# Kernel tuning notes

Measured on AMD Instinct MI355X. Metric: run time of the kernel, lower is better.

Reference implementation:

```python
import jax, jax.numpy as jnp
import numpy as np

N_NODES = 100000
N_EDGES = 640000
D_IN = 128
D_H = 128


def setup_inputs() -> dict:
    key = jax.random.key(0)
    ks = jax.random.split(key, 24)
    def W(k, shp):
        return jax.random.normal(k, shp, dtype=jnp.float32) * 0.05
    inp = {
        "x": jax.random.normal(ks[0], (N_NODES, D_IN), dtype=jnp.float32),
        "src": jax.random.randint(ks[1], (N_EDGES,), 0, N_NODES, dtype=jnp.int32),
        "dst": jax.random.randint(ks[2], (N_EDGES,), 0, N_NODES, dtype=jnp.int32),
        "neg_src": jax.random.randint(ks[3], (N_EDGES,), 0, N_NODES, dtype=jnp.int32),
        "neg_dst": jax.random.randint(ks[4], (N_EDGES,), 0, N_NODES, dtype=jnp.int32),
        # SAGEConv layer 1/2/3: fc_self weight, fc_neigh weight (stored [in,out]), bias
        "Ws1": W(ks[5], (D_IN, D_H)), "Wn1": W(ks[6], (D_IN, D_H)), "b1": jnp.zeros((D_H,), jnp.float32),
        "Ws2": W(ks[7], (D_H, D_H)), "Wn2": W(ks[8], (D_H, D_H)), "b2": jnp.zeros((D_H,), jnp.float32),
        "Ws3": W(ks[9], (D_H, D_H)), "Wn3": W(ks[10], (D_H, D_H)), "b3": jnp.zeros((D_H,), jnp.float32),
        # MLPPredictor: W1 [2h,h], W2 [h,1]
        "Wp1": W(ks[11], (2 * D_H, D_H)), "bp1": jnp.zeros((D_H,), jnp.float32),
        "Wp2": W(ks[12], (D_H, 1)), "bp2": jnp.zeros((1,), jnp.float32),
    }
    return inp


def _sage_mean(x, src, dst, Ws, Wn, b):
    # DGL SAGEConv 'mean': rst = fc_self(h) + fc_neigh(mean_{in-neighbors}(h)) + bias
    n = x.shape[0]
    msum = jax.ops.segment_sum(x[src], dst, num_segments=n)        # [N, d]
    deg = jax.ops.segment_sum(jnp.ones_like(src, dtype=x.dtype), dst, num_segments=n)
    mean = msum / jnp.clip(deg, 1.0)[:, None]                      # zero for isolated nodes
    return x @ Ws + mean @ Wn + b


def _edge_score(h, s, d, Wp1, bp1, Wp2, bp2):
    z = jnp.concatenate([h[s], h[d]], axis=1)                      # [E, 2h]
    return (jax.nn.relu(z @ Wp1 + bp1) @ Wp2 + bp2)[:, 0]          # [E]


def reference(x, src, dst, neg_src, neg_dst,
              Ws1, Wn1, b1, Ws2, Wn2, b2, Ws3, Wn3, b3,
              Wp1, bp1, Wp2, bp2):
    h = _sage_mean(x, src, dst, Ws1, Wn1, b1)
    h = _sage_mean(h, src, dst, Ws2, Wn2, b2)
    h = _sage_mean(h, src, dst, Ws3, Wn3, b3)
    pos = _edge_score(h, src, dst, Wp1, bp1, Wp2, bp2)
    neg = _edge_score(h, neg_src, neg_dst, Wp1, bp1, Wp2, bp2)
    return (pos, neg)
```

## Files before the change

### kernel.cpp

```cpp
#include <hip/hip_runtime.h>

#define N_NODES 100000
#define N_EDGES 640000
#define D 128
#define SCAN_TILE 1024
#define SCAN_BLOCKS ((N_NODES + SCAN_TILE - 1) / SCAN_TILE)

typedef __attribute__((ext_vector_type(8))) short bf16x8;
typedef __attribute__((ext_vector_type(4))) float f32x4;

__device__ __forceinline__ unsigned short f32_to_bf16(float f) {
  union { float f; unsigned int u; } v; v.f = f;
  unsigned int u = v.u;
  unsigned int r = (u + 0x7fffu + ((u >> 16) & 1u)) >> 16;
  return (unsigned short)r;
}
__device__ __forceinline__ float bf16_lo(unsigned int u) { return __uint_as_float(u << 16); }
__device__ __forceinline__ float bf16_hi(unsigned int u) { return __uint_as_float(u & 0xffff0000u); }

__global__ void zero_i32(int* __restrict__ p, int n) {
  int i = blockIdx.x * blockDim.x + threadIdx.x;
  if (i < n) p[i] = 0;
}

__global__ void f32_to_bf16_vec(const float* __restrict__ in, unsigned short* __restrict__ out, int n4) {
  int i = blockIdx.x * blockDim.x + threadIdx.x;
  if (i < n4) {
    float4 v = ((const float4*)in)[i];
    ushort4 o;
    o.x = f32_to_bf16(v.x); o.y = f32_to_bf16(v.y);
    o.z = f32_to_bf16(v.z); o.w = f32_to_bf16(v.w);
    ((ushort4*)out)[i] = o;
  }
}

__global__ void transpose_w(const float* __restrict__ W0, const float* __restrict__ W1,
                            const float* __restrict__ W2, const float* __restrict__ W3,
                            const float* __restrict__ W4, const float* __restrict__ W5,
                            const float* __restrict__ W6, const float* __restrict__ W7,
                            unsigned short* __restrict__ wt) {
  int id = blockIdx.x * 256 + threadIdx.x;
  int mat = id >> 14;
  int rem = id & 16383;
  int n = rem >> 7, k = rem & 127;
  const float* Wm = mat < 4 ? (mat < 2 ? (mat == 0 ? W0 : W1) : (mat == 2 ? W2 : W3))
                            : (mat < 6 ? (mat == 4 ? W4 : W5) : (mat == 6 ? W6 : W7));
  wt[id] = f32_to_bf16(Wm[k * D + n]);
}

__global__ void hist_kernel(const int* __restrict__ dst, int* __restrict__ deg, int E) {
  int i = blockIdx.x * blockDim.x + threadIdx.x;
  if (i < E) atomicAdd(&deg[dst[i]], 1);
}

__global__ void scan_blocksum(const int* __restrict__ deg, int* __restrict__ partial, int n) {
  __shared__ int lds[256];
  const int tid = threadIdx.x;
  const int base = blockIdx.x * SCAN_TILE + tid * 4;
  int s = 0;
#pragma unroll
  for (int j = 0; j < 4; ++j) {
    int i = base + j;
    if (i < n) s += deg[i];
  }
  lds[tid] = s;
  __syncthreads();
  for (int off = 128; off > 0; off >>= 1) {
    if (tid < off) lds[tid] += lds[tid + off];
    __syncthreads();
  }
  if (tid == 0) partial[blockIdx.x] = lds[0];
}

__global__ void scan_offsets(int* __restrict__ partial, int* __restrict__ row_start, int nb, int n) {
  __shared__ int lds[128];
  const int tid = threadIdx.x;
  int v = (tid < nb) ? partial[tid] : 0;
  lds[tid] = v;
  __syncthreads();
  for (int off = 1; off < 128; off <<= 1) {
    int t = (tid >= off) ? lds[tid - off] : 0;
    __syncthreads();
    lds[tid] += t;
    __syncthreads();
  }
  if (tid < nb) partial[tid] = (tid == 0) ? 0 : lds[tid - 1];
  if (tid == 0) row_start[n] = lds[nb - 1];
}

__global__ void scan_final(const int* __restrict__ deg, const int* __restrict__ partial,
                           int* __restrict__ row_start, int n) {
  __shared__ int lds[256];
  const int tid = threadIdx.x;
  const int base = blockIdx.x * SCAN_TILE + tid * 4;
  int d[4];
  int s = 0;
#pragma unroll
  for (int j = 0; j < 4; ++j) {
    int i = base + j;
    d[j] = (i < n) ? deg[i] : 0;
    s += d[j];
  }
  lds[tid] = s;
  __syncthreads();
  for (int off = 1; off < 256; off <<= 1) {
    int t = (tid >= off) ? lds[tid - off] : 0;
    __syncthreads();
    lds[tid] += t;
    __syncthreads();
  }
  int pre = partial[blockIdx.x] + lds[tid] - s;
#pragma unroll
  for (int j = 0; j < 4; ++j) {
    int i = base + j;
    if (i < n) {
      row_start[i] = pre;
      pre += d[j];
    }
  }
}

__global__ void fill_kernel(const int* __restrict__ src, const int* __restrict__ dst,
                            const int* __restrict__ row_start, int* __restrict__ cursor,
                            int* __restrict__ esrc, int E) {
  int i = blockIdx.x * blockDim.x + threadIdx.x;
  if (i < E) {
    int d = dst[i];
    int pos = atomicAdd(&cursor[d], 1);
    esrc[row_start[d] + pos] = src[i];
  }
}

__global__ void aggregate_bf16(const unsigned short* __restrict__ h, const int* __restrict__ row_start,
                               const int* __restrict__ esrc, unsigned short* __restrict__ mean, int n) {
  const int t = blockIdx.x * blockDim.x + threadIdx.x;
  const int node = t >> 4;
  const int fl = threadIdx.x & 15;
  if (node >= n) return;
  const int s0 = row_start[node], s1 = row_start[node + 1];
  float acc[8] = {0.f, 0.f, 0.f, 0.f, 0.f, 0.f, 0.f, 0.f};
  int e = s0;
  for (; e + 4 <= s1; e += 4) {
    int i0 = esrc[e], i1 = esrc[e + 1], i2 = esrc[e + 2], i3 = esrc[e + 3];
    uint4 r0 = *(const uint4*)(h + (size_t)i0 * D + fl * 8);
    uint4 r1 = *(const uint4*)(h + (size_t)i1 * D + fl * 8);
    uint4 r2 = *(const uint4*)(h + (size_t)i2 * D + fl * 8);
    uint4 r3 = *(const uint4*)(h + (size_t)i3 * D + fl * 8);
    acc[0] += bf16_lo(r0.x); acc[1] += bf16_hi(r0.x);
    acc[2] += bf16_lo(r0.y); acc[3] += bf16_hi(r0.y);
    acc[4] += bf16_lo(r0.z); acc[5] += bf16_hi(r0.z);
    acc[6] += bf16_lo(r0.w); acc[7] += bf16_hi(r0.w);
    acc[0] += bf16_lo(r1.x); acc[1] += bf16_hi(r1.x);
    acc[2] += bf16_lo(r1.y); acc[3] += bf16_hi(r1.y);
    acc[4] += bf16_lo(r1.z); acc[5] += bf16_hi(r1.z);
    acc[6] += bf16_lo(r1.w); acc[7] += bf16_hi(r1.w);
    acc[0] += bf16_lo(r2.x); acc[1] += bf16_hi(r2.x);
    acc[2] += bf16_lo(r2.y); acc[3] += bf16_hi(r2.y);
    acc[4] += bf16_lo(r2.z); acc[5] += bf16_hi(r2.z);
    acc[6] += bf16_lo(r2.w); acc[7] += bf16_hi(r2.w);
    acc[0] += bf16_lo(r3.x); acc[1] += bf16_hi(r3.x);
    acc[2] += bf16_lo(r3.y); acc[3] += bf16_hi(r3.y);
    acc[4] += bf16_lo(r3.z); acc[5] += bf16_hi(r3.z);
    acc[6] += bf16_lo(r3.w); acc[7] += bf16_hi(r3.w);
  }
  for (; e < s1; ++e) {
    int s = esrc[e];
    uint4 raw = *(const uint4*)(h + (size_t)s * D + fl * 8);
    acc[0] += bf16_lo(raw.x); acc[1] += bf16_hi(raw.x);
    acc[2] += bf16_lo(raw.y); acc[3] += bf16_hi(raw.y);
    acc[4] += bf16_lo(raw.z); acc[5] += bf16_hi(raw.z);
    acc[6] += bf16_lo(raw.w); acc[7] += bf16_hi(raw.w);
  }
  const float inv = 1.0f / (float)max(s1 - s0, 1);
  uint4 o;
  o.x = (unsigned)f32_to_bf16(acc[0] * inv) | ((unsigned)f32_to_bf16(acc[1] * inv) << 16);
  o.y = (unsigned)f32_to_bf16(acc[2] * inv) | ((unsigned)f32_to_bf16(acc[3] * inv) << 16);
  o.z = (unsigned)f32_to_bf16(acc[4] * inv) | ((unsigned)f32_to_bf16(acc[5] * inv) << 16);
  o.w = (unsigned)f32_to_bf16(acc[6] * inv) | ((unsigned)f32_to_bf16(acc[7] * inv) << 16);
  *(uint4*)(mean + (size_t)node * D + fl * 8) = o;
}

template <int NCHUNK, bool FP32OUT>
__global__ __launch_bounds__(256) void gemm_mfma(
    const unsigned short* __restrict__ in0, const unsigned short* __restrict__ in1,
    const unsigned short* __restrict__ Wt0, const unsigned short* __restrict__ Wt1,
    const float* __restrict__ bias, void* __restrict__ out, int M) {
  __shared__ unsigned short wl[128][136];
  const int tid = threadIdx.x;
  const int lane = tid & 63;
  const int wave = tid >> 6;
  const int m0 = blockIdx.x * 64 + wave * 16;
  const int row = lane & 15;
  const int q = lane >> 4;
  const int mload = min(m0 + row, M - 1);

  bf16x8 afrag[NCHUNK * 4];
#pragma unroll
  for (int s = 0; s < NCHUNK * 4; ++s) {
    const unsigned short* srcp = (NCHUNK == 2 && s >= 4) ? in1 : in0;
    afrag[s] = *reinterpret_cast<const bf16x8*>(srcp + (size_t)mload * D + (s & 3) * 32 + q * 8);
  }
  f32x4 acc[8];
#pragma unroll
  for (int t = 0; t < 8; ++t) acc[t] = (f32x4){0.f, 0.f, 0.f, 0.f};

  for (int c = 0; c < NCHUNK; ++c) {
    const unsigned short* wsrc = (c == 0) ? Wt0 : Wt1;
    if (c) __syncthreads();
#pragma unroll
    for (int i = 0; i < 8; ++i) {
      int seg = i * 256 + tid;
      int r = seg >> 4;
      int o = (seg & 15) * 8;
      *reinterpret_cast<bf16x8*>(&wl[r][o]) =
          *reinterpret_cast<const bf16x8*>(wsrc + r * D + o);
    }
    __syncthreads();
#pragma unroll
    for (int s = 0; s < 4; ++s) {
#pragma unroll
      for (int t = 0; t < 8; ++t) {
        const int n = t * 16 + row;
        bf16x8 b = *reinterpret_cast<const bf16x8*>(&wl[n][s * 32 + q * 8]);
        acc[t] = __builtin_amdgcn_mfma_f32_16x16x32_bf16(afrag[c * 4 + s], b, acc[t], 0, 0, 0);
      }
    }
  }

#pragma unroll
  for (int t = 0; t < 8; ++t) {
    const int col = t * 16 + row;
    const float bv = bias ? bias[col] : 0.f;
#pragma unroll
    for (int r = 0; r < 4; ++r) {
      int m = m0 + q * 4 + r;
      if (m < M) {
        float v = acc[t][r] + bv;
        if (FP32OUT)
          ((float*)out)[(size_t)m * D + col] = v;
        else
          ((unsigned short*)out)[(size_t)m * D + col] = f32_to_bf16(v);
      }
    }
  }
}

__global__ void edge_score_fused(const unsigned short* __restrict__ A, const unsigned short* __restrict__ B,
                                 const int* __restrict__ ps, const int* __restrict__ pd,
                                 const int* __restrict__ ns, const int* __restrict__ nd,
                                 const float* __restrict__ Wp2, const float* __restrict__ bp2,
                                 float* __restrict__ out, int E) {
  const int t = blockIdx.x * blockDim.x + threadIdx.x;
  const int e = t >> 4;
  const int fl = threadIdx.x & 15;
  if (e >= E) return;
  const int si = ps[e], di = pd[e];
  const int nsi = ns[e], ndi = nd[e];
  uint4 ra = *(const uint4*)(A + (size_t)si * D + fl * 8);
  uint4 rb = *(const uint4*)(B + (size_t)di * D + fl * 8);
  uint4 rna = *(const uint4*)(A + (size_t)nsi * D + fl * 8);
  uint4 rnb = *(const uint4*)(B + (size_t)ndi * D + fl * 8);
  float4 w0 = *(const float4*)(Wp2 + fl * 8);
  float4 w1 = *(const float4*)(Wp2 + fl * 8 + 4);

  float pp =
      fmaxf(bf16_lo(ra.x) + bf16_lo(rb.x), 0.f) * w0.x +
      fmaxf(bf16_hi(ra.x) + bf16_hi(rb.x), 0.f) * w0.y +
      fmaxf(bf16_lo(ra.y) + bf16_lo(rb.y), 0.f) * w0.z +
      fmaxf(bf16_hi(ra.y) + bf16_hi(rb.y), 0.f) * w0.w +
      fmaxf(bf16_lo(ra.z) + bf16_lo(rb.z), 0.f) * w1.x +
      fmaxf(bf16_hi(ra.z) + bf16_hi(rb.z), 0.f) * w1.y +
      fmaxf(bf16_lo(ra.w) + bf16_lo(rb.w), 0.f) * w1.z +
      fmaxf(bf16_hi(ra.w) + bf16_hi(rb.w), 0.f) * w1.w;
  float pn =
      fmaxf(bf16_lo(rna.x) + bf16_lo(rnb.x), 0.f) * w0.x +
      fmaxf(bf16_hi(rna.x) + bf16_hi(rnb.x), 0.f) * w0.y +
      fmaxf(bf16_lo(rna.y) + bf16_lo(rnb.y), 0.f) * w0.z +
      fmaxf(bf16_hi(rna.y) + bf16_hi(rnb.y), 0.f) * w0.w +
      fmaxf(bf16_lo(rna.z) + bf16_lo(rnb.z), 0.f) * w1.x +
      fmaxf(bf16_hi(rna.z) + bf16_hi(rnb.z), 0.f) * w1.y +
      fmaxf(bf16_lo(rna.w) + bf16_lo(rnb.w), 0.f) * w1.z +
      fmaxf(bf16_hi(rna.w) + bf16_hi(rnb.w), 0.f) * w1.w;

  pp += __shfl_xor(pp, 1);  pn += __shfl_xor(pn, 1);
  pp += __shfl_xor(pp, 2);  pn += __shfl_xor(pn, 2);
  pp += __shfl_xor(pp, 4);  pn += __shfl_xor(pn, 4);
  pp += __shfl_xor(pp, 8);  pn += __shfl_xor(pn, 8);
  if (fl == 0) {
    float b = bp2[0];
    out[e] = pp + b;
    out[E + e] = pn + b;
  }
}

extern "C" void kernel_launch(void* const* d_in, const int* in_sizes, int n_in,
                              void* d_out, int out_size, void* d_ws, size_t ws_size,
                              hipStream_t stream) {
  const float* x = (const float*)d_in[0];
  const int* src = (const int*)d_in[1];
  const int* dst = (const int*)d_in[2];
  const int* nsrc = (const int*)d_in[3];
  const int* ndst = (const int*)d_in[4];
  const float* Ws1 = (const float*)d_in[5];
  const float* Wn1 = (const float*)d_in[6];
  const float* b1 = (const float*)d_in[7];
  const float* Ws2 = (const float*)d_in[8];
  const float* Wn2 = (const float*)d_in[9];
  const float* b2 = (const float*)d_in[10];
  const float* Ws3 = (const float*)d_in[11];
  const float* Wn3 = (const float*)d_in[12];
  const float* b3 = (const float*)d_in[13];
  const float* Wp1 = (const float*)d_in[14];
  const float* bp1 = (const float*)d_in[15];
  const float* Wp2 = (const float*)d_in[16];
  const float* bp2 = (const float*)d_in[17];
  float* out = (float*)d_out;

  char* ws = (char*)d_ws;
  size_t off = 0;
  auto alloc = [&](size_t bytes) -> void* {
    void* p = ws + off;
    off += (bytes + 255) & ~(size_t)255;
    return p;
  };
  const size_t NODE_F32 = sizeof(float) * (size_t)N_NODES * D;
  char* region0 = (char*)alloc(NODE_F32);
  char* region1 = (char*)alloc(NODE_F32);
  char* region2 = (char*)alloc(NODE_F32);
  int* row_start = (int*)alloc(sizeof(int) * (N_NODES + 1));
  int* deg = (int*)alloc(sizeof(int) * N_NODES * 2);
  int* cursor = deg + N_NODES;
  int* esrc = (int*)alloc(sizeof(int) * N_EDGES);
  int* partial = (int*)alloc(sizeof(int) * 128);
  unsigned short* wt = (unsigned short*)alloc(sizeof(unsigned short) * 8 * D * D);
  (void)ws_size;

  unsigned short* xb = (unsigned short*)region0;
  unsigned short* meanb = xb + (size_t)N_NODES * D;
  unsigned short* hA = (unsigned short*)region1;
  unsigned short* hB = hA + (size_t)N_NODES * D;
  unsigned short* Ab = (unsigned short*)region2;
  unsigned short* Bb = Ab + (size_t)N_NODES * D;

  f32_to_bf16_vec<<<(N_NODES * D / 4 + 255) / 256, 256, 0, stream>>>(x, xb, N_NODES * D / 4);
  transpose_w<<<512, 256, 0, stream>>>(Ws1, Wn1, Ws2, Wn2, Ws3, Wn3, Wp1, Wp1 + D * D, wt);

  zero_i32<<<(2 * N_NODES + 255) / 256, 256, 0, stream>>>(deg, 2 * N_NODES);
  hist_kernel<<<(N_EDGES + 255) / 256, 256, 0, stream>>>(dst, deg, N_EDGES);
  scan_blocksum<<<SCAN_BLOCKS, 256, 0, stream>>>(deg, partial, N_NODES);
  scan_offsets<<<1, 128, 0, stream>>>(partial, row_start, SCAN_BLOCKS, N_NODES);
  scan_final<<<SCAN_BLOCKS, 256, 0, stream>>>(deg, partial, row_start, N_NODES);
  fill_kernel<<<(N_EDGES + 255) / 256, 256, 0, stream>>>(src, dst, row_start, cursor, esrc, N_EDGES);

  const int aggBlocks = (N_NODES * 16 + 255) / 256;
  const int gemmBlocks = (N_NODES + 63) / 64;
  const int edgeBlocks = (N_EDGES * 16) / 256;

  aggregate_bf16<<<aggBlocks, 256, 0, stream>>>(xb, row_start, esrc, meanb, N_NODES);
  gemm_mfma<2, false><<<gemmBlocks, 256, 0, stream>>>(xb, meanb, wt, wt + 16384, b1, hA, N_NODES);
  aggregate_bf16<<<aggBlocks, 256, 0, stream>>>(hA, row_start, esrc, meanb, N_NODES);
  gemm_mfma<2, false><<<gemmBlocks, 256, 0, stream>>>(hA, meanb, wt + 2 * 16384, wt + 3 * 16384, b2, hB, N_NODES);
  aggregate_bf16<<<aggBlocks, 256, 0, stream>>>(hB, row_start, esrc, meanb, N_NODES);
  gemm_mfma<2, false><<<gemmBlocks, 256, 0, stream>>>(hB, meanb, wt + 4 * 16384, wt + 5 * 16384, b3, hA, N_NODES);
  gemm_mfma<1, false><<<gemmBlocks, 256, 0, stream>>>(hA, nullptr, wt + 6 * 16384, nullptr, bp1, Ab, N_NODES);
  gemm_mfma<1, false><<<gemmBlocks, 256, 0, stream>>>(hA, nullptr, wt + 7 * 16384, nullptr, nullptr, Bb, N_NODES);
  edge_score_fused<<<edgeBlocks, 256, 0, stream>>>(Ab, Bb, src, dst, nsrc, ndst, Wp2, bp2, out, N_EDGES);
}
```

Before: 507.5 us.

## Sort edge scoring by destination via dual CSR and fuse predictor GEMMs

The CSR build now covers both positive and negative edges, bucketing negative edges by destination in a second node range and recording an inverse permutation. Edge scoring walks edges in destination-sorted order, so the B-row gathers hit the same or nearby rows, which should improve cache locality. Scores go to a temporary buffer and a permute kernel scatters them back to original order and adds the bias. The two predictor GEMMs are merged into one kernel that loads the A fragments once. In exchange the sort pass does more atomics and writes more memory, and the permute kernel is an extra launch.

```diff
diff --git a/kernel.cpp b/kernel.cpp
--- a/kernel.cpp
+++ b/kernel.cpp
@@ -3,8 +3,10 @@
 #define N_NODES 100000
 #define N_EDGES 640000
 #define D 128
-#define SCAN_TILE 1024
-#define SCAN_BLOCKS ((N_NODES + SCAN_TILE - 1) / SCAN_TILE)
+#define N2 (2 * N_NODES)
+#define E2 (2 * N_EDGES)
+#define SCAN_TILE 2048
+#define SCAN_BLOCKS ((N2 + SCAN_TILE - 1) / SCAN_TILE)
 
 typedef __attribute__((ext_vector_type(8))) short bf16x8;
 typedef __attribute__((ext_vector_type(4))) float f32x4;
@@ -48,18 +50,22 @@
   wt[id] = f32_to_bf16(Wm[k * D + n]);
 }
 
-__global__ void hist_kernel(const int* __restrict__ dst, int* __restrict__ deg, int E) {
+__global__ void hist_dual(const int* __restrict__ dst, const int* __restrict__ ndst,
+                          int* __restrict__ deg, int E) {
   int i = blockIdx.x * blockDim.x + threadIdx.x;
-  if (i < E) atomicAdd(&deg[dst[i]], 1);
+  if (i < E) {
+    atomicAdd(&deg[dst[i]], 1);
+    atomicAdd(&deg[N_NODES + ndst[i]], 1);
+  }
 }
 
 __global__ void scan_blocksum(const int* __restrict__ deg, int* __restrict__ partial, int n) {
   __shared__ int lds[256];
   const int tid = threadIdx.x;
-  const int base = blockIdx.x * SCAN_TILE + tid * 4;
+  const int base = blockIdx.x * SCAN_TILE + tid * 8;
   int s = 0;
 #pragma unroll
-  for (int j = 0; j < 4; ++j) {
+  for (int j = 0; j < 8; ++j) {
     int i = base + j;
     if (i < n) s += deg[i];
   }
@@ -92,11 +98,11 @@
                            int* __restrict__ row_start, int n) {
   __shared__ int lds[256];
   const int tid = threadIdx.x;
-  const int base = blockIdx.x * SCAN_TILE + tid * 4;
-  int d[4];
+  const int base = blockIdx.x * SCAN_TILE + tid * 8;
+  int d[8];
   int s = 0;
 #pragma unroll
-  for (int j = 0; j < 4; ++j) {
+  for (int j = 0; j < 8; ++j) {
     int i = base + j;
     d[j] = (i < n) ? deg[i] : 0;
     s += d[j];
@@ -111,7 +117,7 @@
   }
   int pre = partial[blockIdx.x] + lds[tid] - s;
 #pragma unroll
-  for (int j = 0; j < 4; ++j) {
+  for (int j = 0; j < 8; ++j) {
     int i = base + j;
     if (i < n) {
       row_start[i] = pre;
@@ -120,14 +126,25 @@
   }
 }
 
-__global__ void fill_kernel(const int* __restrict__ src, const int* __restrict__ dst,
-                            const int* __restrict__ row_start, int* __restrict__ cursor,
-                            int* __restrict__ esrc, int E) {
+__global__ void fill_dual(const int* __restrict__ src, const int* __restrict__ dst,
+                          const int* __restrict__ nsrc, const int* __restrict__ ndst,
+                          const int* __restrict__ row_start, int* __restrict__ cursor,
+                          int* __restrict__ esrc, int* __restrict__ edst,
+                          int* __restrict__ inv, int E) {
   int i = blockIdx.x * blockDim.x + threadIdx.x;
   if (i < E) {
     int d = dst[i];
-    int pos = atomicAdd(&cursor[d], 1);
-    esrc[row_start[d] + pos] = src[i];
+    int p = atomicAdd(&cursor[d], 1);
+    int slot = row_start[d] + p;
+    esrc[slot] = src[i];
+    edst[slot] = d;
+    inv[i] = slot;
+    int dn = N_NODES + ndst[i];
+    int p2 = atomicAdd(&cursor[dn], 1);
+    int slot2 = row_start[dn] + p2;
+    esrc[slot2] = nsrc[i];
+    edst[slot2] = ndst[i];
+    inv[E + i] = slot2;
   }
 }
 
@@ -245,52 +262,114 @@
   }
 }
 
-__global__ void edge_score_fused(const unsigned short* __restrict__ A, const unsigned short* __restrict__ B,
-                                 const int* __restrict__ ps, const int* __restrict__ pd,
-                                 const int* __restrict__ ns, const int* __restrict__ nd,
-                                 const float* __restrict__ Wp2, const float* __restrict__ bp2,
-                                 float* __restrict__ out, int E) {
+__global__ __launch_bounds__(256) void gemm_pred(
+    const unsigned short* __restrict__ in,
+    const unsigned short* __restrict__ WtA, const unsigned short* __restrict__ WtB,
+    const float* __restrict__ biasA,
+    unsigned short* __restrict__ outA, unsigned short* __restrict__ outB, int M) {
+  __shared__ unsigned short wl[128][136];
+  const int tid = threadIdx.x;
+  const int lane = tid & 63;
+  const int wave = tid >> 6;
+  const int m0 = blockIdx.x * 64 + wave * 16;
+  const int row = lane & 15;
+  const int q = lane >> 4;
+  const int mload = min(m0 + row, M - 1);
+
+  bf16x8 afrag[4];
+#pragma unroll
+  for (int s = 0; s < 4; ++s)
+    afrag[s] = *reinterpret_cast<const bf16x8*>(in + (size_t)mload * D + s * 32 + q * 8);
+
+  f32x4 acc[8];
+  for (int pass = 0; pass < 2; ++pass) {
+    const unsigned short* wsrc = pass ? WtB : WtA;
+    if (pass) __syncthreads();
+#pragma unroll
+    for (int i = 0; i < 8; ++i) {
+      int seg = i * 256 + tid;
+      int r = seg >> 4;
+      int o = (seg & 15) * 8;
+      *reinterpret_cast<bf16x8*>(&wl[r][o]) =
+          *reinterpret_cast<const bf16x8*>(wsrc + r * D + o);
+    }
+    __syncthreads();
+#pragma unroll
+    for (int t = 0; t < 8; ++t) acc[t] = (f32x4){0.f, 0.f, 0.f, 0.f};
+#pragma unroll
+    for (int s = 0; s < 4; ++s) {
+#pragma unroll
+      for (int t = 0; t < 8; ++t) {
+        const int n = t * 16 + row;
+        bf16x8 b = *reinterpret_cast<const bf16x8*>(&wl[n][s * 32 + q * 8]);
+        acc[t] = __builtin_amdgcn_mfma_f32_16x16x32_bf16(afrag[s], b, acc[t], 0, 0, 0);
+      }
+    }
+    unsigned short* outp = pass ? outB : outA;
+#pragma unroll
+    for (int t = 0; t < 8; ++t) {
+      const int col = t * 16 + row;
+      const float bv = pass ? 0.f : biasA[col];
+#pragma unroll
+      for (int r = 0; r < 4; ++r) {
+        int m = m0 + q * 4 + r;
+        if (m < M) outp[(size_t)m * D + col] = f32_to_bf16(acc[t][r] + bv);
+      }
+    }
+    if (pass == 0) __syncthreads();
+  }
+}
+
+__global__ void edge_score_csr(const unsigned short* __restrict__ A, const unsigned short* __restrict__ B,
+                               const int* __restrict__ esrc, const int* __restrict__ edst,
+                               const float* __restrict__ Wp2, float* __restrict__ tmp, int npairs) {
   const int t = blockIdx.x * blockDim.x + threadIdx.x;
-  const int e = t >> 4;
+  const int g = t >> 4;
   const int fl = threadIdx.x & 15;
-  if (e >= E) return;
-  const int si = ps[e], di = pd[e];
-  const int nsi = ns[e], ndi = nd[e];
-  uint4 ra = *(const uint4*)(A + (size_t)si * D + fl * 8);
-  uint4 rb = *(const uint4*)(B + (size_t)di * D + fl * 8);
-  uint4 rna = *(const uint4*)(A + (size_t)nsi * D + fl * 8);
-  uint4 rnb = *(const uint4*)(B + (size_t)ndi * D + fl * 8);
+  if (g >= npairs) return;
+  const int sl = 2 * g;
+  const int s0 = esrc[sl], d0 = edst[sl];
+  const int s1 = esrc[sl + 1], d1 = edst[sl + 1];
+  uint4 ra0 = *(const uint4*)(A + (size_t)s0 * D + fl * 8);
+  uint4 rb0 = *(const uint4*)(B + (size_t)d0 * D + fl * 8);
+  uint4 ra1 = *(const uint4*)(A + (size_t)s1 * D + fl * 8);
+  uint4 rb1 = *(const uint4*)(B + (size_t)d1 * D + fl * 8);
   float4 w0 = *(const float4*)(Wp2 + fl * 8);
   float4 w1 = *(const float4*)(Wp2 + fl * 8 + 4);
 
-  float pp =
-      fmaxf(bf16_lo(ra.x) + bf16_lo(rb.x), 0.f) * w0.x +
-      fmaxf(bf16_hi(ra.x) + bf16_hi(rb.x), 0.f) * w0.y +
-      fmaxf(bf16_lo(ra.y) + bf16_lo(rb.y), 0.f) * w0.z +
-      fmaxf(bf16_hi(ra.y) + bf16_hi(rb.y), 0.f) * w0.w +
-      fmaxf(bf16_lo(ra.z) + bf16_lo(rb.z), 0.f) * w1.x +
-      fmaxf(bf16_hi(ra.z) + bf16_hi(rb.z), 0.f) * w1.y +
-      fmaxf(bf16_lo(ra.w) + bf16_lo(rb.w), 0.f) * w1.z +
-      fmaxf(bf16_hi(ra.w) + bf16_hi(rb.w), 0.f) * w1.w;
-  float pn =
-      fmaxf(bf16_lo(rna.x) + bf16_lo(rnb.x), 0.f) * w0.x +
-      fmaxf(bf16_hi(rna.x) + bf16_hi(rnb.x), 0.f) * w0.y +
-      fmaxf(bf16_lo(rna.y) + bf16_lo(rnb.y), 0.f) * w0.z +
-      fmaxf(bf16_hi(rna.y) + bf16_hi(rnb.y), 0.f) * w0.w +
-      fmaxf(bf16_lo(rna.z) + bf16_lo(rnb.z), 0.f) * w1.x +
-      fmaxf(bf16_hi(rna.z) + bf16_hi(rnb.z), 0.f) * w1.y +
-      fmaxf(bf16_lo(rna.w) + bf16_lo(rnb.w), 0.f) * w1.z +
-      fmaxf(bf16_hi(rna.w) + bf16_hi(rnb.w), 0.f) * w1.w;
-
-  pp += __shfl_xor(pp, 1);  pn += __shfl_xor(pn, 1);
-  pp += __shfl_xor(pp, 2);  pn += __shfl_xor(pn, 2);
-  pp += __shfl_xor(pp, 4);  pn += __shfl_xor(pn, 4);
-  pp += __shfl_xor(pp, 8);  pn += __shfl_xor(pn, 8);
+  float p0 =
+      fmaxf(bf16_lo(ra0.x) + bf16_lo(rb0.x), 0.f) * w0.x +
+      fmaxf(bf16_hi(ra0.x) + bf16_hi(rb0.x), 0.f) * w0.y +
+      fmaxf(bf16_lo(ra0.y) + bf16_lo(rb0.y), 0.f) * w0.z +
+      fmaxf(bf16_hi(ra0.y) + bf16_hi(rb0.y), 0.f) * w0.w +
+      fmaxf(bf16_lo(ra0.z) + bf16_lo(rb0.z), 0.f) * w1.x +
+      fmaxf(bf16_hi(ra0.z) + bf16_hi(rb0.z), 0.f) * w1.y +
+      fmaxf(bf16_lo(ra0.w) + bf16_lo(rb0.w), 0.f) * w1.z +
+      fmaxf(bf16_hi(ra0.w) + bf16_hi(rb0.w), 0.f) * w1.w;
+  float p1 =
+      fmaxf(bf16_lo(ra1.x) + bf16_lo(rb1.x), 0.f) * w0.x +
+      fmaxf(bf16_hi(ra1.x) + bf16_hi(rb1.x), 0.f) * w0.y +
+      fmaxf(bf16_lo(ra1.y) + bf16_lo(rb1.y), 0.f) * w0.z +
+      fmaxf(bf16_hi(ra1.y) + bf16_hi(rb1.y), 0.f) * w0.w +
+      fmaxf(bf16_lo(ra1.z) + bf16_lo(rb1.z), 0.f) * w1.x +
+      fmaxf(bf16_hi(ra1.z) + bf16_hi(rb1.z), 0.f) * w1.y +
+      fmaxf(bf16_lo(ra1.w) + bf16_lo(rb1.w), 0.f) * w1.z +
+      fmaxf(bf16_hi(ra1.w) + bf16_hi(rb1.w), 0.f) * w1.w;
+
+  p0 += __shfl_xor(p0, 1);  p1 += __shfl_xor(p1, 1);
+  p0 += __shfl_xor(p0, 2);  p1 += __shfl_xor(p1, 2);
+  p0 += __shfl_xor(p0, 4);  p1 += __shfl_xor(p1, 4);
+  p0 += __shfl_xor(p0, 8);  p1 += __shfl_xor(p1, 8);
   if (fl == 0) {
-    float b = bp2[0];
-    out[e] = pp + b;
-    out[E + e] = pn + b;
-  }
+    tmp[sl] = p0;
+    tmp[sl + 1] = p1;
+  }
+}
+
+__global__ void permute_out(const float* __restrict__ tmp, const int* __restrict__ inv,
+                            const float* __restrict__ bp2, float* __restrict__ out, int n) {
+  int i = blockIdx.x * blockDim.x + threadIdx.x;
+  if (i < n) out[i] = tmp[inv[i]] + bp2[0];
 }
 
 extern "C" void kernel_launch(void* const* d_in, const int* in_sizes, int n_in,
@@ -326,12 +405,13 @@
   const size_t NODE_F32 = sizeof(float) * (size_t)N_NODES * D;
   char* region0 = (char*)alloc(NODE_F32);
   char* region1 = (char*)alloc(NODE_F32);
-  char* region2 = (char*)alloc(NODE_F32);
-  int* row_start = (int*)alloc(sizeof(int) * (N_NODES + 1));
-  int* deg = (int*)alloc(sizeof(int) * N_NODES * 2);
-  int* cursor = deg + N_NODES;
-  int* esrc = (int*)alloc(sizeof(int) * N_EDGES);
-  int* partial = (int*)alloc(sizeof(int) * 128);
+  int* row_start = (int*)alloc(sizeof(int) * (N2 + 1));
+  int* deg = (int*)alloc(sizeof(int) * N2 * 2);
+  int* cursor = deg + N2;
+  int* esrc = (int*)alloc(sizeof(int) * E2);
+  int* edst = (int*)alloc(sizeof(int) * E2);
+  int* inv = (int*)alloc(sizeof(int) * E2);
+  int* partial = (int*)alloc(sizeof(int) * 256);
   unsigned short* wt = (unsigned short*)alloc(sizeof(unsigned short) * 8 * D * D);
   (void)ws_size;
 
@@ -339,22 +419,23 @@
   unsigned short* meanb = xb + (size_t)N_NODES * D;
   unsigned short* hA = (unsigned short*)region1;
   unsigned short* hB = hA + (size_t)N_NODES * D;
-  unsigned short* Ab = (unsigned short*)region2;
-  unsigned short* Bb = Ab + (size_t)N_NODES * D;
+  unsigned short* Ab = xb;
+  unsigned short* Bb = meanb;
+  float* tmp = (float*)hB;
 
   f32_to_bf16_vec<<<(N_NODES * D / 4 + 255) / 256, 256, 0, stream>>>(x, xb, N_NODES * D / 4);
   transpose_w<<<512, 256, 0, stream>>>(Ws1, Wn1, Ws2, Wn2, Ws3, Wn3, Wp1, Wp1 + D * D, wt);
 
-  zero_i32<<<(2 * N_NODES + 255) / 256, 256, 0, stream>>>(deg, 2 * N_NODES);
-  hist_kernel<<<(N_EDGES + 255) / 256, 256, 0, stream>>>(dst, deg, N_EDGES);
-  scan_blocksum<<<SCAN_BLOCKS, 256, 0, stream>>>(deg, partial, N_NODES);
-  scan_offsets<<<1, 128, 0, stream>>>(partial, row_start, SCAN_BLOCKS, N_NODES);
-  scan_final<<<SCAN_BLOCKS, 256, 0, stream>>>(deg, partial, row_start, N_NODES);
-  fill_kernel<<<(N_EDGES + 255) / 256, 256, 0, stream>>>(src, dst, row_start, cursor, esrc, N_EDGES);
+  zero_i32<<<(2 * N2 + 255) / 256, 256, 0, stream>>>(deg, 2 * N2);
+  hist_dual<<<(N_EDGES + 255) / 256, 256, 0, stream>>>(dst, ndst, deg, N_EDGES);
+  scan_blocksum<<<SCAN_BLOCKS, 256, 0, stream>>>(deg, partial, N2);
+  scan_offsets<<<1, 128, 0, stream>>>(partial, row_start, SCAN_BLOCKS, N2);
+  scan_final<<<SCAN_BLOCKS, 256, 0, stream>>>(deg, partial, row_start, N2);
+  fill_dual<<<(N_EDGES + 255) / 256, 256, 0, stream>>>(src, dst, nsrc, ndst, row_start, cursor,
+                                                       esrc, edst, inv, N_EDGES);
 
   const int aggBlocks = (N_NODES * 16 + 255) / 256;
   const int gemmBlocks = (N_NODES + 63) / 64;
-  const int edgeBlocks = (N_EDGES * 16) / 256;
 
   aggregate_bf16<<<aggBlocks, 256, 0, stream>>>(xb, row_start, esrc, meanb, N_NODES);
   gemm_mfma<2, false><<<gemmBlocks, 256, 0, stream>>>(xb, meanb, wt, wt + 16384, b1, hA, N_NODES);
@@ -362,7 +443,7 @@
   gemm_mfma<2, false><<<gemmBlocks, 256, 0, stream>>>(hA, meanb, wt + 2 * 16384, wt + 3 * 16384, b2, hB, N_NODES);
   aggregate_bf16<<<aggBlocks, 256, 0, stream>>>(hB, row_start, esrc, meanb, N_NODES);
   gemm_mfma<2, false><<<gemmBlocks, 256, 0, stream>>>(hB, meanb, wt + 4 * 16384, wt + 5 * 16384, b3, hA, N_NODES);
-  gemm_mfma<1, false><<<gemmBlocks, 256, 0, stream>>>(hA, nullptr, wt + 6 * 16384, nullptr, bp1, Ab, N_NODES);
-  gemm_mfma<1, false><<<gemmBlocks, 256, 0, stream>>>(hA, nullptr, wt + 7 * 16384, nullptr, nullptr, Bb, N_NODES);
-  edge_score_fused<<<edgeBlocks, 256, 0, stream>>>(Ab, Bb, src, dst, nsrc, ndst, Wp2, bp2, out, N_EDGES);
-}
+  gemm_pred<<<gemmBlocks, 256, 0, stream>>>(hA, wt + 6 * 16384, wt + 7 * 16384, bp1, Ab, Bb, N_NODES);
+  edge_score_csr<<<(N_EDGES * 16 + 255) / 256, 256, 0, stream>>>(Ab, Bb, esrc, edst, Wp2, tmp, N_EDGES);
+  permute_out<<<(E2 + 255) / 256, 256, 0, stream>>>(tmp, inv, bp2, out, E2);
+}
```

Measured after the change: 536.5 us. 5.7% more time.

## Use wave-per-node aggregation and fuse the two predictor GEMMs

Applied to the files above, without the earlier changes.

The mean aggregation now gives each node a full 64-lane wave: four 16-lane groups each take every fourth edge, and the partial sums are combined with cross-lane shuffles before one group writes the result. This is meant to expose more memory-level parallelism per node than the old 16-lane scheme with its 4-way unrolled loop, at the cost of idle lanes for low-degree nodes. The two predictor projections are merged into one kernel that loads the A-fragments once and runs two passes over different weight tiles, saving one launch and one read of the hidden state. Both predictor outputs now reuse the input buffers, so one workspace region is no longer allocated.

```diff
diff --git a/kernel.cpp b/kernel.cpp
--- a/kernel.cpp
+++ b/kernel.cpp
@@ -131,39 +131,16 @@
   }
 }
 
-__global__ void aggregate_bf16(const unsigned short* __restrict__ h, const int* __restrict__ row_start,
+__global__ void aggregate_wave(const unsigned short* __restrict__ h, const int* __restrict__ row_start,
                                const int* __restrict__ esrc, unsigned short* __restrict__ mean, int n) {
-  const int t = blockIdx.x * blockDim.x + threadIdx.x;
-  const int node = t >> 4;
-  const int fl = threadIdx.x & 15;
+  const int node = (blockIdx.x * blockDim.x + threadIdx.x) >> 6;
+  const int lane = threadIdx.x & 63;
   if (node >= n) return;
+  const int q = lane >> 4;
+  const int fl = lane & 15;
   const int s0 = row_start[node], s1 = row_start[node + 1];
   float acc[8] = {0.f, 0.f, 0.f, 0.f, 0.f, 0.f, 0.f, 0.f};
-  int e = s0;
-  for (; e + 4 <= s1; e += 4) {
-    int i0 = esrc[e], i1 = esrc[e + 1], i2 = esrc[e + 2], i3 = esrc[e + 3];
-    uint4 r0 = *(const uint4*)(h + (size_t)i0 * D + fl * 8);
-    uint4 r1 = *(const uint4*)(h + (size_t)i1 * D + fl * 8);
-    uint4 r2 = *(const uint4*)(h + (size_t)i2 * D + fl * 8);
-    uint4 r3 = *(const uint4*)(h + (size_t)i3 * D + fl * 8);
-    acc[0] += bf16_lo(r0.x); acc[1] += bf16_hi(r0.x);
-    acc[2] += bf16_lo(r0.y); acc[3] += bf16_hi(r0.y);
-    acc[4] += bf16_lo(r0.z); acc[5] += bf16_hi(r0.z);
-    acc[6] += bf16_lo(r0.w); acc[7] += bf16_hi(r0.w);
-    acc[0] += bf16_lo(r1.x); acc[1] += bf16_hi(r1.x);
-    acc[2] += bf16_lo(r1.y); acc[3] += bf16_hi(r1.y);
-    acc[4] += bf16_lo(r1.z); acc[5] += bf16_hi(r1.z);
-    acc[6] += bf16_lo(r1.w); acc[7] += bf16_hi(r1.w);
-    acc[0] += bf16_lo(r2.x); acc[1] += bf16_hi(r2.x);
-    acc[2] += bf16_lo(r2.y); acc[3] += bf16_hi(r2.y);
-    acc[4] += bf16_lo(r2.z); acc[5] += bf16_hi(r2.z);
-    acc[6] += bf16_lo(r2.w); acc[7] += bf16_hi(r2.w);
-    acc[0] += bf16_lo(r3.x); acc[1] += bf16_hi(r3.x);
-    acc[2] += bf16_lo(r3.y); acc[3] += bf16_hi(r3.y);
-    acc[4] += bf16_lo(r3.z); acc[5] += bf16_hi(r3.z);
-    acc[6] += bf16_lo(r3.w); acc[7] += bf16_hi(r3.w);
-  }
-  for (; e < s1; ++e) {
+  for (int e = s0 + q; e < s1; e += 4) {
     int s = esrc[e];
     uint4 raw = *(const uint4*)(h + (size_t)s * D + fl * 8);
     acc[0] += bf16_lo(raw.x); acc[1] += bf16_hi(raw.x);
@@ -171,13 +148,20 @@
     acc[4] += bf16_lo(raw.z); acc[5] += bf16_hi(raw.z);
     acc[6] += bf16_lo(raw.w); acc[7] += bf16_hi(raw.w);
   }
-  const float inv = 1.0f / (float)max(s1 - s0, 1);
-  uint4 o;
-  o.x = (unsigned)f32_to_bf16(acc[0] * inv) | ((unsigned)f32_to_bf16(acc[1] * inv) << 16);
-  o.y = (unsigned)f32_to_bf16(acc[2] * inv) | ((unsigned)f32_to_bf16(acc[3] * inv) << 16);
-  o.z = (unsigned)f32_to_bf16(acc[4] * inv) | ((unsigned)f32_to_bf16(acc[5] * inv) << 16);
-  o.w = (unsigned)f32_to_bf16(acc[6] * inv) | ((unsigned)f32_to_bf16(acc[7] * inv) << 16);
-  *(uint4*)(mean + (size_t)node * D + fl * 8) = o;
+#pragma unroll
+  for (int j = 0; j < 8; ++j) {
+    acc[j] += __shfl_xor(acc[j], 16);
+    acc[j] += __shfl_xor(acc[j], 32);
+  }
+  if (q == 0) {
+    const float inv = 1.0f / (float)max(s1 - s0, 1);
+    uint4 o;
+    o.x = (unsigned)f32_to_bf16(acc[0] * inv) | ((unsigned)f32_to_bf16(acc[1] * inv) << 16);
+    o.y = (unsigned)f32_to_bf16(acc[2] * inv) | ((unsigned)f32_to_bf16(acc[3] * inv) << 16);
+    o.z = (unsigned)f32_to_bf16(acc[4] * inv) | ((unsigned)f32_to_bf16(acc[5] * inv) << 16);
+    o.w = (unsigned)f32_to_bf16(acc[6] * inv) | ((unsigned)f32_to_bf16(acc[7] * inv) << 16);
+    *(uint4*)(mean + (size_t)node * D + fl * 8) = o;
+  }
 }
 
 template <int NCHUNK, bool FP32OUT>
@@ -242,6 +226,64 @@
           ((unsigned short*)out)[(size_t)m * D + col] = f32_to_bf16(v);
       }
     }
+  }
+}
+
+__global__ __launch_bounds__(256) void gemm_pred(
+    const unsigned short* __restrict__ in,
+    const unsigned short* __restrict__ WtA, const unsigned short* __restrict__ WtB,
+    const float* __restrict__ biasA,
+    unsigned short* __restrict__ outA, unsigned short* __restrict__ outB, int M) {
+  __shared__ unsigned short wl[128][136];
+  const int tid = threadIdx.x;
+  const int lane = tid & 63;
+  const int wave = tid >> 6;
+  const int m0 = blockIdx.x * 64 + wave * 16;
+  const int row = lane & 15;
+  const int q = lane >> 4;
+  const int mload = min(m0 + row, M - 1);
+
+  bf16x8 afrag[4];
+#pragma unroll
+  for (int s = 0; s < 4; ++s)
+    afrag[s] = *reinterpret_cast<const bf16x8*>(in + (size_t)mload * D + s * 32 + q * 8);
+
+  f32x4 acc[8];
+  for (int pass = 0; pass < 2; ++pass) {
+    const unsigned short* wsrc = pass ? WtB : WtA;
+    if (pass) __syncthreads();
+#pragma unroll
+    for (int i = 0; i < 8; ++i) {
+      int seg = i * 256 + tid;
+      int r = seg >> 4;
+      int o = (seg & 15) * 8;
+      *reinterpret_cast<bf16x8*>(&wl[r][o]) =
+          *reinterpret_cast<const bf16x8*>(wsrc + r * D + o);
+    }
+    __syncthreads();
+#pragma unroll
+    for (int t = 0; t < 8; ++t) acc[t] = (f32x4){0.f, 0.f, 0.f, 0.f};
+#pragma unroll
+    for (int s = 0; s < 4; ++s) {
+#pragma unroll
+      for (int t = 0; t < 8; ++t) {
+        const int n = t * 16 + row;
+        bf16x8 b = *reinterpret_cast<const bf16x8*>(&wl[n][s * 32 + q * 8]);
+        acc[t] = __builtin_amdgcn_mfma_f32_16x16x32_bf16(afrag[s], b, acc[t], 0, 0, 0);
+      }
+    }
+    unsigned short* outp = pass ? outB : outA;
+#pragma unroll
+    for (int t = 0; t < 8; ++t) {
+      const int col = t * 16 + row;
+      const float bv = pass ? 0.f : biasA[col];
+#pragma unroll
+      for (int r = 0; r < 4; ++r) {
+        int m = m0 + q * 4 + r;
+        if (m < M) outp[(size_t)m * D + col] = f32_to_bf16(acc[t][r] + bv);
+      }
+    }
+    if (pass == 0) __syncthreads();
   }
 }
 
@@ -326,7 +368,6 @@
   const size_t NODE_F32 = sizeof(float) * (size_t)N_NODES * D;
   char* region0 = (char*)alloc(NODE_F32);
   char* region1 = (char*)alloc(NODE_F32);
-  char* region2 = (char*)alloc(NODE_F32);
   int* row_start = (int*)alloc(sizeof(int) * (N_NODES + 1));
   int* deg = (int*)alloc(sizeof(int) * N_NODES * 2);
   int* cursor = deg + N_NODES;
@@ -339,8 +380,8 @@
   unsigned short* meanb = xb + (size_t)N_NODES * D;
   unsigned short* hA = (unsigned short*)region1;
   unsigned short* hB = hA + (size_t)N_NODES * D;
-  unsigned short* Ab = (unsigned short*)region2;
-  unsigned short* Bb = Ab + (size_t)N_NODES * D;
+  unsigned short* Ab = xb;
+  unsigned short* Bb = meanb;
 
   f32_to_bf16_vec<<<(N_NODES * D / 4 + 255) / 256, 256, 0, stream>>>(x, xb, N_NODES * D / 4);
   transpose_w<<<512, 256, 0, stream>>>(Ws1, Wn1, Ws2, Wn2, Ws3, Wn3, Wp1, Wp1 + D * D, wt);
@@ -352,17 +393,16 @@
   scan_final<<<SCAN_BLOCKS, 256, 0, stream>>>(deg, partial, row_start, N_NODES);
   fill_kernel<<<(N_EDGES + 255) / 256, 256, 0, stream>>>(src, dst, row_start, cursor, esrc, N_EDGES);
 
-  const int aggBlocks = (N_NODES * 16 + 255) / 256;
+  const int aggBlocks = (N_NODES * 64 + 255) / 256;
   const int gemmBlocks = (N_NODES + 63) / 64;
   const int edgeBlocks = (N_EDGES * 16) / 256;
 
-  aggregate_bf16<<<aggBlocks, 256, 0, stream>>>(xb, row_start, esrc, meanb, N_NODES);
+  aggregate_wave<<<aggBlocks, 256, 0, stream>>>(xb, row_start, esrc, meanb, N_NODES);
   gemm_mfma<2, false><<<gemmBlocks, 256, 0, stream>>>(xb, meanb, wt, wt + 16384, b1, hA, N_NODES);
-  aggregate_bf16<<<aggBlocks, 256, 0, stream>>>(hA, row_start, esrc, meanb, N_NODES);
+  aggregate_wave<<<aggBlocks, 256, 0, stream>>>(hA, row_start, esrc, meanb, N_NODES);
   gemm_mfma<2, false><<<gemmBlocks, 256, 0, stream>>>(hA, meanb, wt + 2 * 16384, wt + 3 * 16384, b2, hB, N_NODES);
-  aggregate_bf16<<<aggBlocks, 256, 0, stream>>>(hB, row_start, esrc, meanb, N_NODES);
+  aggregate_wave<<<aggBlocks, 256, 0, stream>>>(hB, row_start, esrc, meanb, N_NODES);
   gemm_mfma<2, false><<<gemmBlocks, 256, 0, stream>>>(hB, meanb, wt + 4 * 16384, wt + 5 * 16384, b3, hA, N_NODES);
-  gemm_mfma<1, false><<<gemmBlocks, 256, 0, stream>>>(hA, nullptr, wt + 6 * 16384, nullptr, bp1, Ab, N_NODES);
-  gemm_mfma<1, false><<<gemmBlocks, 256, 0, stream>>>(hA, nullptr, wt + 7 * 16384, nullptr, nullptr, Bb, N_NODES);
+  gemm_pred<<<gemmBlocks, 256, 0, stream>>>(hA, wt + 6 * 16384, wt + 7 * 16384, bp1, Ab, Bb, N_NODES);
   edge_score_fused<<<edgeBlocks, 256, 0, stream>>>(Ab, Bb, src, dst, nsrc, ndst, Wp2, bp2, out, N_EDGES);
 }
```

After: 514.1 us. Within noise of the previous version (+1.3%).
